# Optimization experiments

Measured on AMD Instinct MI355X. Metric: run time of the kernel, lower is better.

## Reference

```python
import jax, jax.numpy as jnp
import numpy as np

B, N, C = 16, 577, 768
H, D = 12, 64
HID = 3072
EPS = 1e-5


def setup_inputs() -> dict:
    key = jax.random.key(0)
    ks = jax.random.split(key, 5)
    s = 0.02
    return {
        "x": jax.random.normal(ks[0], (B, N, C), jnp.float32),
        "w_qkv": jax.random.normal(ks[1], (C, 3 * C), jnp.float32) * s,
        "b_qkv": jnp.zeros((3 * C,), jnp.float32),
        "w_proj": jax.random.normal(ks[2], (C, C), jnp.float32) * s,
        "b_proj": jnp.zeros((C,), jnp.float32),
        "g1": jnp.ones((C,), jnp.float32),
        "be1": jnp.zeros((C,), jnp.float32),
        "g2": jnp.ones((C,), jnp.float32),
        "be2": jnp.zeros((C,), jnp.float32),
        "w1": jax.random.normal(ks[3], (C, HID), jnp.float32) * s,
        "b1": jnp.zeros((HID,), jnp.float32),
        "w2": jax.random.normal(ks[4], (HID, C), jnp.float32) * s,
        "b2": jnp.zeros((C,), jnp.float32),
    }


def _layernorm(x, g, b):
    mu = jnp.mean(x, axis=-1, keepdims=True)
    var = jnp.mean(jnp.square(x - mu), axis=-1, keepdims=True)
    return (x - mu) * jax.lax.rsqrt(var + EPS) * g + b


def reference(x, w_qkv, b_qkv, w_proj, b_proj, g1, be1, g2, be2, w1, b1, w2, b2):
    # --- pre-norm MHA ---
    xn = _layernorm(x, g1, be1)
    qkv = xn @ w_qkv + b_qkv                      # [B,N,3C]
    qkv = qkv.reshape(B, N, 3, H, D).transpose(2, 0, 3, 1, 4)  # [3,B,H,N,D]
    q, k, v = qkv[0], qkv[1], qkv[2]
    scale = 1.0 / jnp.sqrt(jnp.float32(D))
    scores = jnp.einsum("bhnd,bhmd->bhnm", q, k) * scale
    attn_weights = jax.nn.softmax(scores, axis=-1)  # [B,H,N,N]
    ctx = jnp.einsum("bhnm,bhmd->bhnd", attn_weights, v)
    ctx = ctx.transpose(0, 2, 1, 3).reshape(B, N, C)
    attn_out = ctx @ w_proj + b_proj
    x = x + attn_out
    # --- MLP (exact GELU, matching nn.GELU default) ---
    h = _layernorm(x, g2, be2) @ w1 + b1
    h = jax.nn.gelu(h, approximate=False)
    x = x + (h @ w2 + b2)
    return x, attn_weights
```

## Files before the change

### kernel.cpp

```cpp
#include <hip/hip_runtime.h>
#include <hip/hip_bf16.h>
#include <cmath>

constexpr int B_ = 16, N_ = 577, C_ = 768, H_ = 12, D_ = 64, HID_ = 3072;
constexpr int ROWS_ = B_ * N_;
constexpr int BH_ = B_ * H_;
constexpr int KVT_ = 10;
constexpr int QBLK_ = 10;

typedef __attribute__((ext_vector_type(8))) __bf16 bf16x8;
typedef __attribute__((ext_vector_type(4))) float f32x4;
typedef __attribute__((ext_vector_type(4), aligned(4))) float f32x4u;

#define DEVI __device__ __forceinline__

DEVI unsigned short f2bf(float f) {
  unsigned u = __float_as_uint(f);
  return (unsigned short)((u + 0x7fffu + ((u >> 16) & 1u)) >> 16);
}

DEVI void gload16(const void* src, void* dst) {
  __builtin_amdgcn_global_load_lds(
      (const __attribute__((address_space(1))) char*)src,
      (__attribute__((address_space(3))) char*)dst, 16, 0, 0);
}
#define VMCNT0 asm volatile("s_waitcnt vmcnt(0)" ::: "memory")
#define VMW(n) asm volatile("s_waitcnt vmcnt(" #n ")" ::: "memory")
#define FENCE asm volatile("" ::: "memory")
#define RAWBAR do { FENCE; __builtin_amdgcn_s_barrier(); FENCE; } while (0)

__global__ __launch_bounds__(256) void cvtT_kernel(const float* __restrict__ in,
                                                   unsigned short* __restrict__ out,
                                                   int K, int N) {
  __shared__ float t[64][65];
  int n0 = blockIdx.x * 64, k0 = blockIdx.y * 64;
  int tx = threadIdx.x & 63, ty = threadIdx.x >> 6;
#pragma unroll
  for (int r = 0; r < 16; r++) {
    int kr = ty * 16 + r;
    t[kr][tx] = in[(long)(k0 + kr) * N + n0 + tx];
  }
  __syncthreads();
#pragma unroll
  for (int r = 0; r < 16; r++) {
    int nr = ty * 16 + r;
    out[(long)(n0 + nr) * K + k0 + tx] = f2bf(t[tx][nr]);
  }
}

__global__ __launch_bounds__(256) void ln_kernel(const float* __restrict__ x,
                                                 const float* __restrict__ g,
                                                 const float* __restrict__ be,
                                                 unsigned short* __restrict__ out) {
  int row = blockIdx.x;
  const float* xr = x + (long)row * C_;
  float v[3];
  float s = 0.f, s2 = 0.f;
#pragma unroll
  for (int j = 0; j < 3; j++) {
    int i = threadIdx.x + j * 256;
    v[j] = xr[i];
    s += v[j];
    s2 += v[j] * v[j];
  }
#pragma unroll
  for (int o = 32; o > 0; o >>= 1) {
    s += __shfl_down(s, o);
    s2 += __shfl_down(s2, o);
  }
  __shared__ float sh[8];
  int w = threadIdx.x >> 6;
  if ((threadIdx.x & 63) == 0) { sh[w] = s; sh[4 + w] = s2; }
  __syncthreads();
  s = sh[0] + sh[1] + sh[2] + sh[3];
  s2 = sh[4] + sh[5] + sh[6] + sh[7];
  float mu = s * (1.f / C_);
  float var = s2 * (1.f / C_) - mu * mu;
  float rs = rsqrtf(var + 1e-5f);
#pragma unroll
  for (int j = 0; j < 3; j++) {
    int i = threadIdx.x + j * 256;
    out[(long)row * C_ + i] = f2bf((v[j] - mu) * rs * g[i] + be[i]);
  }
}

__global__ __launch_bounds__(256) void attn_kernel(
    const unsigned short* __restrict__ qg,
    const unsigned short* __restrict__ kg,
    const unsigned short* __restrict__ vt,
    float* __restrict__ attn,
    unsigned short* __restrict__ ctx,
    float* __restrict__ dump) {
  __shared__ unsigned short Ks[2][64][64];
  __shared__ unsigned short Vs[2][64][64];
  __shared__ unsigned short Ps[4][16][40];
  const int wgid = (blockIdx.x & 7) * (BH_ * QBLK_ / 8) + (blockIdx.x >> 3);
  const int bh = wgid / QBLK_, qb = wgid % QBLK_;
  const int b = bh / H_, h = bh % H_;
  const int tid = threadIdx.x, wave = tid >> 6, lane = tid & 63;
  const int l15 = lane & 15, l4 = lane >> 4;
  const int q0w = qb * 64 + wave * 16;

  const unsigned short* Qh = qg + (long)bh * N_ * D_;
  const char* Kb = (const char*)(kg + (long)bh * N_ * D_);
  const char* Vb = (const char*)(vt + (long)bh * D_ * N_);

  int qrc = q0w + l15; if (qrc >= N_) qrc = N_ - 1;
  bf16x8 qa0 = *(const bf16x8*)(Qh + (long)qrc * D_ + l4 * 8);
  bf16x8 qa1 = *(const bf16x8*)(Qh + (long)qrc * D_ + 32 + l4 * 8);

  auto srcAddr = [&](const char* g0, long rstride, int i) -> const char* {
    int off = i * 4096 + tid * 16;
    int row = off >> 7, colD = off & 127;
    return g0 + (long)row * rstride + (colD ^ ((row & 7) << 4));
  };
  auto stageK = [&](int bu, int kt) {
    const char* g0 = Kb + (long)kt * 8192;
#pragma unroll
    for (int i = 0; i < 2; i++)
      gload16(srcAddr(g0, 128, i), ((char*)Ks) + bu * 8192 + i * 4096 + wave * 1024);
  };
  auto stageV = [&](int bu, int kt) {
    const char* g0 = Vb + (long)kt * 128;
#pragma unroll
    for (int i = 0; i < 2; i++)
      gload16(srcAddr(g0, (long)N_ * 2, i), ((char*)Vs) + bu * 8192 + i * 4096 + wave * 1024);
  };
  auto rdK = [&](int bu, int row, int colb) -> bf16x8 {
    return *(const bf16x8*)(((const char*)Ks) + bu * 8192 + row * 128 +
                            (colb ^ ((row & 7) << 4)));
  };
  auto rdV = [&](int bu, int row, int colb) -> bf16x8 {
    return *(const bf16x8*)(((const char*)Vs) + bu * 8192 + row * 128 +
                            (colb ^ ((row & 7) << 4)));
  };
  auto computeS = [&](int bu, f32x4 (&s)[4]) {
#pragma unroll
    for (int nf = 0; nf < 4; nf++) {
      int row = nf * 16 + l15;
      bf16x8 k0v = rdK(bu, row, l4 * 16);
      bf16x8 k1v = rdK(bu, row, 64 + l4 * 16);
      f32x4 z = {0.f, 0.f, 0.f, 0.f};
      z = __builtin_amdgcn_mfma_f32_16x16x32_bf16(k0v, qa0, z, 0, 0, 0);
      z = __builtin_amdgcn_mfma_f32_16x16x32_bf16(k1v, qa1, z, 0, 0, 0);
      s[nf] = z;
    }
  };
  auto maskLast = [&](f32x4 (&s)[4]) {
#pragma unroll
    for (int nf = 0; nf < 4; nf++)
#pragma unroll
      for (int r = 0; r < 4; r++) {
        if (nf == 0 && r == 0)
          s[nf][r] = (l4 == 0) ? s[nf][r] : -1e30f;
        else
          s[nf][r] = -1e30f;
      }
  };

  float m_ln = -1e30f, l_ln = 0.f;
  stageK(0, 0);
#pragma unroll
  for (int kt = 0; kt < KVT_; kt++) {
    VMCNT0; RAWBAR;
    if (kt + 1 < KVT_) stageK((kt + 1) & 1, kt + 1);
    f32x4 s[4];
    computeS(kt & 1, s);
    if (kt == KVT_ - 1) maskLast(s);
    float mt = s[0][0];
#pragma unroll
    for (int nf = 0; nf < 4; nf++)
#pragma unroll
      for (int r = 0; r < 4; r++) mt = fmaxf(mt, s[nf][r]);
    float mn = fmaxf(m_ln, mt);
    float acc = 0.f;
#pragma unroll
    for (int nf = 0; nf < 4; nf++)
#pragma unroll
      for (int r = 0; r < 4; r++) acc += __expf(s[nf][r] - mn);
    l_ln = l_ln * __expf(m_ln - mn) + acc;
    m_ln = mn;
  }

  RAWBAR;
  stageK(0, 0); stageV(0, 0);

  float m = fmaxf(m_ln, __shfl_xor(m_ln, 16));
  m = fmaxf(m, __shfl_xor(m, 32));
  float lr = l_ln * __expf(m_ln - m);
  lr += __shfl_xor(lr, 16);
  lr += __shfl_xor(lr, 32);
  float inv_l = 1.f / lr;

  f32x4 cacc[4];
#pragma unroll
  for (int nf = 0; nf < 4; nf++) cacc[nf] = f32x4{0.f, 0.f, 0.f, 0.f};

  const int qv = q0w + l15;
  const bool qok = qv < N_;
  float* prow = attn + ((long)bh * N_ + (qok ? qv : 0)) * N_;

#pragma unroll
  for (int kt = 0; kt < KVT_; kt++) {
    const int bu = kt & 1;
    if (kt == 0) { VMW(0); } else { VMW(4); }
    RAWBAR;
    if (kt + 1 < KVT_) { stageK((kt + 1) & 1, kt + 1); stageV((kt + 1) & 1, kt + 1); }
    f32x4 s[4];
    computeS(bu, s);
    if (kt == KVT_ - 1) maskLast(s);
    float p[4][4];
#pragma unroll
    for (int nf = 0; nf < 4; nf++)
#pragma unroll
      for (int r = 0; r < 4; r++) p[nf][r] = __expf(s[nf][r] - m) * inv_l;

    if (kt < KVT_ - 1) {
#pragma unroll
      for (int nf = 0; nf < 4; nf++) {
        f32x4u val;
        val[0] = p[nf][0]; val[1] = p[nf][1]; val[2] = p[nf][2]; val[3] = p[nf][3];
        float* a = qok ? (prow + kt * 64 + nf * 16 + l4 * 4) : (dump + tid * 4);
        *(f32x4u*)a = val;
      }
    } else {
      float* a = (qok && l4 == 0) ? (prow + 576) : (dump + tid);
      *a = p[0][0];
    }

#pragma unroll
    for (int nf = 0; nf < 4; nf++) {
      unsigned lo = (__float_as_uint(p[nf][1]) & 0xffff0000u) |
                    (__float_as_uint(p[nf][0]) >> 16);
      unsigned hi = (__float_as_uint(p[nf][3]) & 0xffff0000u) |
                    (__float_as_uint(p[nf][2]) >> 16);
      *(uint2*)&Ps[wave][l15][nf * 16 + l4 * 4] = uint2{lo, hi};
    }
#pragma unroll
    for (int ks = 0; ks < 2; ks++) {
      bf16x8 pa = *(const bf16x8*)&Ps[wave][l15][ks * 32 + l4 * 8];
#pragma unroll
      for (int nf = 0; nf < 4; nf++) {
        bf16x8 vb = rdV(bu, nf * 16 + l15, ks * 64 + l4 * 16);
        cacc[nf] = __builtin_amdgcn_mfma_f32_16x16x32_bf16(pa, vb, cacc[nf], 0, 0, 0);
      }
    }
  }

#pragma unroll
  for (int nf = 0; nf < 4; nf++)
#pragma unroll
    for (int r = 0; r < 4; r++) {
      int qw = q0w + l4 * 4 + r;
      if (qw >= N_) continue;
      int d = nf * 16 + l15;
      ctx[((long)b * N_ + qw) * C_ + h * D_ + d] = f2bf(cacc[nf][r]);
    }
}

template <int EPI>
__global__ __launch_bounds__(256) void gemm128(
    const unsigned short* __restrict__ A,
    const unsigned short* __restrict__ BT,
    int M, int K, int Nc,
    void* __restrict__ outp, const float* __restrict__ bias,
    const float* __restrict__ resid) {
  __shared__ unsigned short As[2][128][64];
  __shared__ unsigned short Bs[2][128][64];
  const int tid = threadIdx.x, wave = tid >> 6, lane = tid & 63;
  const int l15 = lane & 15, l4 = lane >> 4;
  const long m0 = (long)blockIdx.y * 128, n0 = (long)blockIdx.x * 128;
  const int wr = (wave >> 1) * 64, wc = (wave & 1) * 64;

  f32x4 acc[4][4];
#pragma unroll
  for (int i = 0; i < 4; i++)
#pragma unroll
    for (int j = 0; j < 4; j++) acc[i][j] = f32x4{0.f, 0.f, 0.f, 0.f};

  auto stageA = [&](int buf, int t) {
#pragma unroll
    for (int i = 0; i < 4; i++) {
      int off = i * 4096 + tid * 16;
      int row = off >> 7, colD = off & 127;
      long gr = m0 + row; if (gr >= M) gr = M - 1;
      const char* src = (const char*)A + (gr * (long)K + (long)t * 64) * 2 +
                        (colD ^ ((row & 7) << 4));
      char* dst = ((char*)As) + buf * 16384 + i * 4096 + wave * 1024;
      gload16(src, dst);
    }
  };
  auto stageB = [&](int buf, int t) {
#pragma unroll
    for (int i = 0; i < 4; i++) {
      int off = i * 4096 + tid * 16;
      int row = off >> 7, colD = off & 127;
      const char* src = (const char*)BT + ((n0 + row) * (long)K + (long)t * 64) * 2 +
                        (colD ^ ((row & 7) << 4));
      char* dst = ((char*)Bs) + buf * 16384 + i * 4096 + wave * 1024;
      gload16(src, dst);
    }
  };

  const int nt = K / 64;
  stageA(0, 0); stageB(0, 0);
  VMCNT0; __syncthreads();
  int buf = 0;
  for (int t = 0; t < nt; t++) {
    if (t + 1 < nt) { stageA(buf ^ 1, t + 1); stageB(buf ^ 1, t + 1); }
    bf16x8 af[4][2], bfr[4][2];
#pragma unroll
    for (int mf = 0; mf < 4; mf++)
#pragma unroll
      for (int kk = 0; kk < 2; kk++) {
        int row = wr + mf * 16 + l15, colb = kk * 64 + l4 * 16;
        af[mf][kk] = *(const bf16x8*)(((const char*)As) + buf * 16384 + row * 128 +
                                      (colb ^ ((row & 7) << 4)));
      }
#pragma unroll
    for (int nf = 0; nf < 4; nf++)
#pragma unroll
      for (int kk = 0; kk < 2; kk++) {
        int row = wc + nf * 16 + l15, colb = kk * 64 + l4 * 16;
        bfr[nf][kk] = *(const bf16x8*)(((const char*)Bs) + buf * 16384 + row * 128 +
                                       (colb ^ ((row & 7) << 4)));
      }
#pragma unroll
    for (int kk = 0; kk < 2; kk++)
#pragma unroll
      for (int mf = 0; mf < 4; mf++)
#pragma unroll
        for (int nf = 0; nf < 4; nf++)
          acc[mf][nf] =
              __builtin_amdgcn_mfma_f32_16x16x32_bf16(af[mf][kk], bfr[nf][kk], acc[mf][nf], 0, 0, 0);
    VMCNT0; __syncthreads();
    buf ^= 1;
  }

#pragma unroll
  for (int mf = 0; mf < 4; mf++)
#pragma unroll
    for (int nf = 0; nf < 4; nf++)
#pragma unroll
      for (int r = 0; r < 4; r++) {
        long row = m0 + wr + mf * 16 + l4 * 4 + r;
        long col = n0 + wc + nf * 16 + l15;
        if (row >= M) continue;
        float v = acc[mf][nf][r];
        if constexpr (EPI == 3 || EPI == 5) {
          float* o = (float*)outp;
          long idx = row * (long)Nc + col;
          o[idx] = v + bias[col] + resid[idx];
        } else if constexpr (EPI == 4) {
          v += bias[col];
          float ge = 0.5f * v * (1.f + erff(v * 0.70710678118654752f));
          ((unsigned short*)outp)[row * (long)Nc + col] = f2bf(ge);
        }
      }
}

template <int EPI>
__global__ __launch_bounds__(512, 2) void gemm256(
    const unsigned short* __restrict__ A,
    const unsigned short* __restrict__ BT,
    int M, int K, int Nc,
    void* __restrict__ outp, const float* __restrict__ bias,
    const float* __restrict__ resid) {
  __shared__ unsigned short smem[2][2][2][128][64];
  const int tid = threadIdx.x, wave = tid >> 6, lane = tid & 63;
  const int l15 = lane & 15, l4 = lane >> 4;
  const int wm = wave >> 2, wn = wave & 3;

  const int nbx = gridDim.x;
  const int nwg = nbx * gridDim.y;
  int orig = blockIdx.y * nbx + blockIdx.x;
  int qq = nwg >> 3, r8 = nwg & 7;
  int xcd = orig & 7, idx = orig >> 3;
  int wg = (xcd < r8 ? xcd * (qq + 1) : r8 * (qq + 1) + (xcd - r8) * qq) + idx;
  const long m0 = (long)(wg / nbx) * 256;
  const long n0 = (long)(wg % nbx) * 256;

  f32x4 acc[2][2][4][2];
#pragma unroll
  for (int a = 0; a < 2; a++)
#pragma unroll
    for (int b = 0; b < 2; b++)
#pragma unroll
      for (int m = 0; m < 4; m++)
#pragma unroll
        for (int n = 0; n < 2; n++) acc[a][b][m][n] = f32x4{0.f, 0.f, 0.f, 0.f};

  auto stage = [&](int d, int op, int half, int t) {
#pragma unroll
    for (int it = 0; it < 2; it++) {
      int off = it * 8192 + tid * 16;
      int lrow = off >> 7, colb = off & 127;
      long grow;
      if (op == 0) {
        grow = m0 + half * 128 + lrow;
        if (grow >= M) grow = M - 1;
      } else {
        grow = n0 + half * 128 + lrow;
      }
      const unsigned short* gp = (op == 0) ? A : BT;
      const char* src = (const char*)(gp + grow * (long)K + (long)t * 64) +
                        (colb ^ ((lrow & 7) << 4));
      char* dst = ((char*)smem) + (((d * 2 + op) * 2 + half) * 16384) + off;
      gload16(src, dst);
    }
  };
  auto rdfrag = [&](int d, int op, int half, int lr, int kk) -> bf16x8 {
    const char* p = ((const char*)smem) + (((d * 2 + op) * 2 + half) * 16384) + lr * 128 +
                    ((kk * 64 + l4 * 16) ^ ((lr & 7) << 4));
    return *(const bf16x8*)p;
  };

  bf16x8 av[4][2];

#define PHASE(d, qm, qn, STAGECODE, VMCODE)                                              \
  {                                                                                      \
    if constexpr (qn == 0) {                                                             \
      _Pragma("unroll") for (int m = 0; m < 4; m++)                                      \
          _Pragma("unroll") for (int kk = 0; kk < 2; kk++)                               \
              av[m][kk] = rdfrag(d, 0, qm, wm * 64 + m * 16 + l15, kk);                  \
    }                                                                                    \
    bf16x8 bv[2][2];                                                                     \
    _Pragma("unroll") for (int n = 0; n < 2; n++)                                        \
        _Pragma("unroll") for (int kk = 0; kk < 2; kk++)                                 \
            bv[n][kk] = rdfrag(d, 1, qn, wn * 32 + n * 16 + l15, kk);                    \
    STAGECODE;                                                                           \
    VMCODE;                                                                              \
    RAWBAR;                                                                              \
    __builtin_amdgcn_s_setprio(1);                                                       \
    _Pragma("unroll") for (int kk = 0; kk < 2; kk++)                                     \
        _Pragma("unroll") for (int m = 0; m < 4; m++)                                    \
            _Pragma("unroll") for (int n = 0; n < 2; n++)                                \
                acc[qm][qn][m][n] = __builtin_amdgcn_mfma_f32_16x16x32_bf16(             \
                    av[m][kk], bv[n][kk], acc[qm][qn][m][n], 0, 0, 0);                   \
    __builtin_amdgcn_s_setprio(0);                                                       \
    RAWBAR;                                                                              \
  }

  const int nt = K / 64, ni = nt / 2;
  stage(0, 0, 0, 0); stage(0, 0, 1, 0); stage(0, 1, 0, 0); stage(0, 1, 1, 0);
  stage(1, 0, 0, 1); stage(1, 0, 1, 1); stage(1, 1, 0, 1); stage(1, 1, 1, 1);
  asm volatile("s_waitcnt vmcnt(8)" ::: "memory");
  RAWBAR;

  for (int i = 0; i < ni; i++) {
    const int t1 = 2 * i + 1, t2 = 2 * i + 2, t3 = 2 * i + 3;
    PHASE(0, 0, 0, { if (i > 0) stage(1, 0, 1, t1); }, {});
    PHASE(0, 0, 1, { if (i > 0) stage(1, 1, 1, t1); }, {});
    PHASE(0, 1, 0, { if (t2 < nt) stage(0, 0, 0, t2); }, {});
    PHASE(0, 1, 1, { if (t2 < nt) stage(0, 1, 0, t2); },
          { if (t2 < nt) { asm volatile("s_waitcnt vmcnt(4)" ::: "memory"); }
            else { asm volatile("s_waitcnt vmcnt(0)" ::: "memory"); } });
    PHASE(1, 0, 0, { if (t2 < nt) stage(0, 0, 1, t2); }, {});
    PHASE(1, 0, 1, { if (t2 < nt) stage(0, 1, 1, t2); }, {});
    PHASE(1, 1, 0, { if (t3 < nt) stage(1, 0, 0, t3); }, {});
    PHASE(1, 1, 1, { if (t3 < nt) stage(1, 1, 0, t3); },
          { if (t3 < nt) { asm volatile("s_waitcnt vmcnt(4)" ::: "memory"); }
            else { asm volatile("s_waitcnt vmcnt(0)" ::: "memory"); } });
  }
#undef PHASE

#pragma unroll
  for (int qm = 0; qm < 2; qm++)
#pragma unroll
    for (int qn = 0; qn < 2; qn++)
#pragma unroll
      for (int m = 0; m < 4; m++)
#pragma unroll
        for (int n = 0; n < 2; n++)
#pragma unroll
          for (int r = 0; r < 4; r++) {
            long row = m0 + qm * 128 + wm * 64 + m * 16 + l4 * 4 + r;
            long col = n0 + qn * 128 + wn * 32 + n * 16 + l15;
            if (row >= M) continue;
            float v = acc[qm][qn][m][n][r];
            if constexpr (EPI == 0) {
              v += bias[col];
              int which = (int)col / C_;
              int rem = (int)col % C_;
              int hh = rem >> 6, d = rem & 63;
              int bb = (int)row / N_, nn = (int)row % N_;
              if (which == 0) v *= 0.125f;
              unsigned short* o = (unsigned short*)outp;
              long base = (long)which * ((long)BH_ * N_ * D_);
              long oidx;
              if (which < 2)
                oidx = base + (((long)(bb * H_ + hh)) * N_ + nn) * D_ + d;
              else
                oidx = base + (((long)(bb * H_ + hh)) * D_ + d) * N_ + nn;
              o[oidx] = f2bf(v);
            } else if constexpr (EPI == 4) {
              v += bias[col];
              float ge = 0.5f * v * (1.f + erff(v * 0.70710678118654752f));
              ((unsigned short*)outp)[row * (long)Nc + col] = f2bf(ge);
            } else {
              float* o = (float*)outp;
              long oidx = row * (long)Nc + col;
              o[oidx] = v + bias[col] + resid[oidx];
            }
          }
}

extern "C" void kernel_launch(void* const* d_in, const int* in_sizes, int n_in,
                              void* d_out, int out_size, void* d_ws, size_t ws_size,
                              hipStream_t stream) {
  const float* x = (const float*)d_in[0];
  const float* w_qkv = (const float*)d_in[1];
  const float* b_qkv = (const float*)d_in[2];
  const float* w_proj = (const float*)d_in[3];
  const float* b_proj = (const float*)d_in[4];
  const float* g1 = (const float*)d_in[5];
  const float* be1 = (const float*)d_in[6];
  const float* g2 = (const float*)d_in[7];
  const float* be2 = (const float*)d_in[8];
  const float* w1 = (const float*)d_in[9];
  const float* b1 = (const float*)d_in[10];
  const float* w2 = (const float*)d_in[11];
  const float* b2 = (const float*)d_in[12];

  char* ws = (char*)d_ws;
  const size_t SZ_TOK_BF = (size_t)ROWS_ * C_ * 2;
  unsigned short* xn = (unsigned short*)(ws);
  unsigned short* q = (unsigned short*)(ws + SZ_TOK_BF);
  unsigned short* v = (unsigned short*)(ws + 3 * SZ_TOK_BF);
  unsigned short* ctx = (unsigned short*)(ws + 4 * SZ_TOK_BF);
  unsigned short* hbuf = q;
  float* x1 = (float*)(ws + 5 * SZ_TOK_BF);
  unsigned short* wqkvT = (unsigned short*)(ws + 5 * SZ_TOK_BF + (size_t)ROWS_ * C_ * 4);
  unsigned short* wprojT = wqkvT + (size_t)C_ * 3 * C_;
  unsigned short* w1T = wprojT + (size_t)C_ * C_;
  unsigned short* w2T = w1T + (size_t)C_ * HID_;
  float* dump = (float*)(w2T + (size_t)HID_ * C_);

  float* out_x = (float*)d_out;
  float* attn = out_x + (size_t)ROWS_ * C_;

  cvtT_kernel<<<dim3(3 * C_ / 64, C_ / 64), 256, 0, stream>>>(w_qkv, wqkvT, C_, 3 * C_);
  cvtT_kernel<<<dim3(C_ / 64, C_ / 64), 256, 0, stream>>>(w_proj, wprojT, C_, C_);
  cvtT_kernel<<<dim3(HID_ / 64, C_ / 64), 256, 0, stream>>>(w1, w1T, C_, HID_);
  cvtT_kernel<<<dim3(C_ / 64, HID_ / 64), 256, 0, stream>>>(w2, w2T, HID_, C_);

  ln_kernel<<<ROWS_, 256, 0, stream>>>(x, g1, be1, xn);

  {
    dim3 g(3 * C_ / 256, (ROWS_ + 255) / 256);
    gemm256<0><<<g, 512, 0, stream>>>(xn, wqkvT, ROWS_, C_, 3 * C_, q, b_qkv, nullptr);
  }
  attn_kernel<<<BH_ * QBLK_, 256, 0, stream>>>(q, q + (size_t)BH_ * N_ * D_, v, attn, ctx,
                                               dump);
  {
    dim3 g(C_ / 128, (ROWS_ + 127) / 128);
    gemm128<3><<<g, 256, 0, stream>>>(ctx, wprojT, ROWS_, C_, C_, x1, b_proj, x);
  }
  ln_kernel<<<ROWS_, 256, 0, stream>>>(x1, g2, be2, xn);
  {
    dim3 g(HID_ / 256, (ROWS_ + 255) / 256);
    gemm256<4><<<g, 512, 0, stream>>>(xn, w1T, ROWS_, C_, HID_, hbuf, b1, nullptr);
  }
  {
    dim3 g(C_ / 128, (ROWS_ + 127) / 128);
    gemm128<5><<<g, 256, 0, stream>>>(hbuf, w2T, ROWS_, HID_, C_, out_x, b2, x1);
  }
}
```

Before: 491.2 us.

## Triple-buffer attention K/V loads, relax GEMM waits, merge weight conversion kernels

The attention kernel moves from double to triple buffering of its K and V tiles in LDS. It prefetches two tiles ahead and uses partial vmcnt waits, so global loads overlap more of the compute. In the gemm128 loop, the next tile is now issued before a partial wait, which replaces the full wait and __syncthreads at the end of each iteration. The four weight transpose/convert launches become a single launch that dispatches on block index. The cost is more LDS per attention block, which may lower occupancy, and more fragile wait-count bookkeeping.

```diff
diff --git a/kernel.cpp b/kernel.cpp
--- a/kernel.cpp
+++ b/kernel.cpp
@@ -29,11 +29,19 @@
 #define FENCE asm volatile("" ::: "memory")
 #define RAWBAR do { FENCE; __builtin_amdgcn_s_barrier(); FENCE; } while (0)
 
-__global__ __launch_bounds__(256) void cvtT_kernel(const float* __restrict__ in,
-                                                   unsigned short* __restrict__ out,
-                                                   int K, int N) {
+__global__ __launch_bounds__(256) void cvtAll_kernel(
+    const float* __restrict__ a0, unsigned short* __restrict__ o0,
+    const float* __restrict__ a1, unsigned short* __restrict__ o1,
+    const float* __restrict__ a2, unsigned short* __restrict__ o2,
+    const float* __restrict__ a3, unsigned short* __restrict__ o3) {
   __shared__ float t[64][65];
-  int n0 = blockIdx.x * 64, k0 = blockIdx.y * 64;
+  int bid = blockIdx.x;
+  const float* in; unsigned short* out; int K, N, nx;
+  if (bid < 432) { in = a0; out = o0; K = 768; N = 2304; nx = 36; }
+  else if (bid < 576) { bid -= 432; in = a1; out = o1; K = 768; N = 768; nx = 12; }
+  else if (bid < 1152) { bid -= 576; in = a2; out = o2; K = 768; N = 3072; nx = 48; }
+  else { bid -= 1152; in = a3; out = o3; K = 3072; N = 768; nx = 12; }
+  int n0 = (bid % nx) * 64, k0 = (bid / nx) * 64;
   int tx = threadIdx.x & 63, ty = threadIdx.x >> 6;
 #pragma unroll
   for (int r = 0; r < 16; r++) {
@@ -91,8 +99,8 @@
     float* __restrict__ attn,
     unsigned short* __restrict__ ctx,
     float* __restrict__ dump) {
-  __shared__ unsigned short Ks[2][64][64];
-  __shared__ unsigned short Vs[2][64][64];
+  __shared__ unsigned short Ks[3][64][64];
+  __shared__ unsigned short Vs[3][64][64];
   __shared__ unsigned short Ps[4][16][40];
   const int wgid = (blockIdx.x & 7) * (BH_ * QBLK_ / 8) + (blockIdx.x >> 3);
   const int bh = wgid / QBLK_, qb = wgid % QBLK_;
@@ -159,13 +167,14 @@
   };
 
   float m_ln = -1e30f, l_ln = 0.f;
-  stageK(0, 0);
+  stageK(0, 0); stageK(1, 1);
 #pragma unroll
   for (int kt = 0; kt < KVT_; kt++) {
-    VMCNT0; RAWBAR;
-    if (kt + 1 < KVT_) stageK((kt + 1) & 1, kt + 1);
+    if (kt < KVT_ - 1) { VMW(2); } else { VMW(0); }
+    RAWBAR;
+    if (kt + 2 < KVT_) stageK((kt + 2) % 3, kt + 2);
     f32x4 s[4];
-    computeS(kt & 1, s);
+    computeS(kt % 3, s);
     if (kt == KVT_ - 1) maskLast(s);
     float mt = s[0][0];
 #pragma unroll
@@ -183,7 +192,7 @@
   }
 
   RAWBAR;
-  stageK(0, 0); stageV(0, 0);
+  stageK(0, 0); stageV(0, 0); stageK(1, 1); stageV(1, 1);
 
   float m = fmaxf(m_ln, __shfl_xor(m_ln, 16));
   m = fmaxf(m, __shfl_xor(m, 32));
@@ -202,10 +211,13 @@
 
 #pragma unroll
   for (int kt = 0; kt < KVT_; kt++) {
-    const int bu = kt & 1;
-    if (kt == 0) { VMW(0); } else { VMW(4); }
+    const int bu = kt % 3;
+    if (kt == 0) { VMW(4); }
+    else if (kt == 1) { VMW(8); }
+    else if (kt < KVT_ - 1) { VMW(12); }
+    else { VMW(8); }
     RAWBAR;
-    if (kt + 1 < KVT_) { stageK((kt + 1) & 1, kt + 1); stageV((kt + 1) & 1, kt + 1); }
+    if (kt + 2 < KVT_) { stageK((kt + 2) % 3, kt + 2); stageV((kt + 2) % 3, kt + 2); }
     f32x4 s[4];
     computeS(bu, s);
     if (kt == KVT_ - 1) maskLast(s);
@@ -304,10 +316,15 @@
 
   const int nt = K / 64;
   stageA(0, 0); stageB(0, 0);
-  VMCNT0; __syncthreads();
   int buf = 0;
   for (int t = 0; t < nt; t++) {
-    if (t + 1 < nt) { stageA(buf ^ 1, t + 1); stageB(buf ^ 1, t + 1); }
+    if (t + 1 < nt) {
+      stageA(buf ^ 1, t + 1); stageB(buf ^ 1, t + 1);
+      VMW(8);
+    } else {
+      VMCNT0;
+    }
+    RAWBAR;
     bf16x8 af[4][2], bfr[4][2];
 #pragma unroll
     for (int mf = 0; mf < 4; mf++)
@@ -333,7 +350,7 @@
         for (int nf = 0; nf < 4; nf++)
           acc[mf][nf] =
               __builtin_amdgcn_mfma_f32_16x16x32_bf16(af[mf][kk], bfr[nf][kk], acc[mf][nf], 0, 0, 0);
-    VMCNT0; __syncthreads();
+    RAWBAR;
     buf ^= 1;
   }
 
@@ -539,10 +556,7 @@
   float* out_x = (float*)d_out;
   float* attn = out_x + (size_t)ROWS_ * C_;
 
-  cvtT_kernel<<<dim3(3 * C_ / 64, C_ / 64), 256, 0, stream>>>(w_qkv, wqkvT, C_, 3 * C_);
-  cvtT_kernel<<<dim3(C_ / 64, C_ / 64), 256, 0, stream>>>(w_proj, wprojT, C_, C_);
-  cvtT_kernel<<<dim3(HID_ / 64, C_ / 64), 256, 0, stream>>>(w1, w1T, C_, HID_);
-  cvtT_kernel<<<dim3(C_ / 64, HID_ / 64), 256, 0, stream>>>(w2, w2T, HID_, C_);
+  cvtAll_kernel<<<1728, 256, 0, stream>>>(w_qkv, wqkvT, w_proj, wprojT, w1, w1T, w2, w2T);
 
   ln_kernel<<<ROWS_, 256, 0, stream>>>(x, g1, be1, xn);
 
```

Measured after the change: 481.6 us. No clear change (-2.0%).
